# Kernel optimization log

Measured on AMD Instinct MI355X. Metric: run time of the kernel, lower is better.

## Reference

```python
import jax, jax.numpy as jnp
import numpy as np

C_IN = 256


def setup_inputs() -> dict:
    key = jax.random.key(0)
    ks = jax.random.split(key, 10)
    B, C, H, W = 1, C_IN, 96, 96
    Cq = C // 8
    s = 0.05
    return {
        "x": jax.random.normal(ks[0], (B, C, H, W), dtype=jnp.float32),
        "Wq": jax.random.normal(ks[1], (Cq, C), dtype=jnp.float32) * s,
        "bq": jax.random.normal(ks[2], (Cq,), dtype=jnp.float32) * s,
        "Wk": jax.random.normal(ks[3], (Cq, C), dtype=jnp.float32) * s,
        "bk": jax.random.normal(ks[4], (Cq,), dtype=jnp.float32) * s,
        "Wv": jax.random.normal(ks[5], (C, C), dtype=jnp.float32) * s,
        "bv": jax.random.normal(ks[6], (C,), dtype=jnp.float32) * s,
        "W6": jax.random.normal(ks[7], (C, C), dtype=jnp.float32) * s,
        "b6": jax.random.normal(ks[8], (C,), dtype=jnp.float32) * s,
        "gamma": jnp.ones((1,), dtype=jnp.float32),
    }


def reference(x, Wq, bq, Wk, bk, Wv, bv, W6, b6, gamma):
    # TRM forward (OFS just wraps it). 1x1 convs expressed as einsums.
    B, C, H, W = x.shape
    N = H * W
    scale = C ** -0.5  # 1 / sqrt(in_dim)
    xf = x.reshape(B, C, N)
    q = jnp.einsum('oc,bcn->bon', Wq, xf) + bq[None, :, None]   # (B, C/8, N)
    k = jnp.einsum('oc,bcn->bon', Wk, xf) + bk[None, :, None]   # (B, C/8, N)
    v = jnp.einsum('oc,bcn->bon', Wv, xf) + bv[None, :, None]   # (B, C,   N)
    # energy[b,n,m] = sum_c q[b,c,n] * k[b,c,m]  -> full spatial attention (B,N,N)
    energy = jnp.einsum('bcn,bcm->bnm', q, k)
    att = jax.nn.softmax(energy, axis=-1)
    # out[b,c,n] = sum_m v[b,c,m] * att[b,n,m]
    out = jnp.einsum('bcm,bnm->bcn', v, att)                    # (B, C, N)
    # torch: out.permute(2,0,1) -> (N,B,C); max/mean over C; sum; mean over B
    out_co = out.max(axis=1) + out.mean(axis=1)                 # (B, N)
    x_co = out_co.mean(axis=0).reshape(B, -1) * scale           # valid because B == 1
    x_co = jax.nn.softmax(x_co, axis=-1).reshape(B, 1, H, W)    # spatial gate
    gated = x * x_co
    y = jnp.einsum('oc,bchw->bohw', W6, gated) + b6[None, :, None, None]
    return gamma * y + x + y
```

## Files before the change

kernel.cpp:

```cpp
#include <hip/hip_runtime.h>

#define N 9216
#define CIN 256
#define DQ 32
#define NT 144
#define LOG2E 1.44269504088896340736f

typedef short short8 __attribute__((ext_vector_type(8)));
typedef float floatx4 __attribute__((ext_vector_type(4)));
typedef unsigned short ushort_t;

__device__ __forceinline__ ushort_t f2bf(float f) {
  union { float f; unsigned u; } a; a.f = f;
  unsigned u = a.u;
  u += 0x7fffu + ((u >> 16) & 1u);
  return (ushort_t)(u >> 16);
}
__device__ __forceinline__ float bf2f(ushort_t h) {
  union { unsigned u; float f; } a; a.u = ((unsigned)h) << 16;
  return a.f;
}

__global__ __launch_bounds__(256) void qkv_kernel(
    const float* __restrict__ x,
    const float* __restrict__ Wq, const float* __restrict__ bq,
    const float* __restrict__ Wk, const float* __restrict__ bk,
    const float* __restrict__ Wv, const float* __restrict__ bv,
    ushort_t* __restrict__ qT, ushort_t* __restrict__ kT,
    ushort_t* __restrict__ vG)
{
  __shared__ float xs[64][68];
  const int t = threadIdx.x;
  const int n0 = blockIdx.x * 64;
  const int oc = blockIdx.y;
  const int i = t >> 4, j = t & 15;
  const int o0 = oc * 64 + i * 4;

  const float* Wrow[4];
  float bias[4];
#pragma unroll
  for (int r = 0; r < 4; ++r) {
    const int o = o0 + r;
    if (oc == 0) {
      if (o < 32) { Wrow[r] = Wq + o * CIN;        bias[r] = bq[o]; }
      else        { Wrow[r] = Wk + (o - 32) * CIN; bias[r] = bk[o - 32]; }
    } else        { Wrow[r] = Wv + (o - 64) * CIN; bias[r] = bv[o - 64]; }
  }

  float acc[4][4] = {};
  for (int cc = 0; cc < 4; ++cc) {
    {
      const int row = t >> 2, cq = t & 3;
      const float* src = x + (size_t)(cc * 64 + row) * N + n0 + cq * 16;
      float4 a0 = *(const float4*)(src + 0);
      float4 a1 = *(const float4*)(src + 4);
      float4 a2 = *(const float4*)(src + 8);
      float4 a3 = *(const float4*)(src + 12);
      float* dst = &xs[row][cq * 16];
      *(float4*)(dst + 0) = a0; *(float4*)(dst + 4)  = a1;
      *(float4*)(dst + 8) = a2; *(float4*)(dst + 12) = a3;
    }
    __syncthreads();
#pragma unroll 2
    for (int k4 = 0; k4 < 16; ++k4) {
      float4 wv4[4];
#pragma unroll
      for (int r = 0; r < 4; ++r)
        wv4[r] = *(const float4*)(Wrow[r] + cc * 64 + k4 * 4);
#pragma unroll
      for (int kk = 0; kk < 4; ++kk) {
        float4 xv = *(const float4*)&xs[k4 * 4 + kk][j * 4];
#pragma unroll
        for (int r = 0; r < 4; ++r) {
          const float wval = ((const float*)&wv4[r])[kk];
          acc[r][0] += wval * xv.x;
          acc[r][1] += wval * xv.y;
          acc[r][2] += wval * xv.z;
          acc[r][3] += wval * xv.w;
        }
      }
    }
    __syncthreads();
  }

#pragma unroll
  for (int r = 0; r < 4; ++r) {
    const int o = o0 + r;
#pragma unroll
    for (int c = 0; c < 4; ++c) {
      const int n = n0 + j * 4 + c;
      const float val = acc[r][c] + bias[r];
      if (oc == 0) {
        if (o < 32) qT[(size_t)n * DQ + o]        = f2bf(val * LOG2E);
        else        kT[(size_t)n * DQ + (o - 32)] = f2bf(val);
      } else        vG[(size_t)(o - 64) * N + n]  = f2bf(val);
    }
  }
}

__global__ __launch_bounds__(256, 2) void attn_kernel(
    const ushort_t* __restrict__ qT, const ushort_t* __restrict__ kT,
    const ushort_t* __restrict__ vG,
    ushort_t* __restrict__ Opart, float* __restrict__ lpart,
    int sliceIters)
{
  __shared__ ushort_t Pb[2][64][36];

  const int t = threadIdx.x;
  const int w = t >> 6;
  const int lane = t & 63;
  const int quad = lane >> 4;
  const int l15 = lane & 15;
  const int nt = blockIdx.x;
  const int s  = blockIdx.y;
  const int n0 = nt * 64;
  const int mbase = s * sliceIters * 32;
  const int cw = w * 64;

  short8 aq = *(const short8*)(qT + (size_t)(n0 + 16 * w + l15) * DQ + 8 * quad);

  floatx4 acc[4][4];
#pragma unroll
  for (int a2 = 0; a2 < 4; ++a2)
#pragma unroll
    for (int b2 = 0; b2 < 4; ++b2)
      acc[a2][b2] = (floatx4){0.f, 0.f, 0.f, 0.f};
  float lsum[4] = {0.f, 0.f, 0.f, 0.f};
  const floatx4 z4 = {0.f, 0.f, 0.f, 0.f};

  for (int it = 0; it < sliceIters; ++it) {
    const int m0 = mbase + it * 32;

    short8 kb0 = *(const short8*)(kT + (size_t)(m0 + l15) * DQ + 8 * quad);
    short8 kb1 = *(const short8*)(kT + (size_t)(m0 + 16 + l15) * DQ + 8 * quad);
    floatx4 s0 = __builtin_amdgcn_mfma_f32_16x16x32_bf16(aq, kb0, z4, 0, 0, 0);
    floatx4 s1 = __builtin_amdgcn_mfma_f32_16x16x32_bf16(aq, kb1, z4, 0, 0, 0);

    const ushort_t* vb = vG + (size_t)m0 + 8 * quad;
    short8 av0 = *(const short8*)(vb + (size_t)(cw +  0 + l15) * N);
    short8 av1 = *(const short8*)(vb + (size_t)(cw + 16 + l15) * N);
    short8 av2 = *(const short8*)(vb + (size_t)(cw + 32 + l15) * N);
    short8 av3 = *(const short8*)(vb + (size_t)(cw + 48 + l15) * N);

    ushort_t* pb = &Pb[it & 1][0][0];
#pragma unroll
    for (int r = 0; r < 4; ++r) {
      float p0 = exp2f(s0[r]);
      float p1 = exp2f(s1[r]);
      lsum[r] += p0 + p1;
      const int row = 16 * w + 4 * quad + r;
      pb[row * 36 + l15]      = f2bf(p0);
      pb[row * 36 + 16 + l15] = f2bf(p1);
    }
    __syncthreads();

#pragma unroll
    for (int b2 = 0; b2 < 4; ++b2) {
      const ushort_t* pr = pb + (b2 * 16 + l15) * 36 + 8 * quad;
      union { uint2 u2[2]; short8 v; } u;
      u.u2[0] = *(const uint2*)(pr);
      u.u2[1] = *(const uint2*)(pr + 4);
      const short8 pf = u.v;
      acc[0][b2] = __builtin_amdgcn_mfma_f32_16x16x32_bf16(av0, pf, acc[0][b2], 0, 0, 0);
      acc[1][b2] = __builtin_amdgcn_mfma_f32_16x16x32_bf16(av1, pf, acc[1][b2], 0, 0, 0);
      acc[2][b2] = __builtin_amdgcn_mfma_f32_16x16x32_bf16(av2, pf, acc[2][b2], 0, 0, 0);
      acc[3][b2] = __builtin_amdgcn_mfma_f32_16x16x32_bf16(av3, pf, acc[3][b2], 0, 0, 0);
    }
  }

#pragma unroll
  for (int r = 0; r < 4; ++r) {
    float v = lsum[r];
    v += __shfl_xor(v, 1);
    v += __shfl_xor(v, 2);
    v += __shfl_xor(v, 4);
    v += __shfl_xor(v, 8);
    lsum[r] = v;
  }
  if (l15 == 0) {
#pragma unroll
    for (int r = 0; r < 4; ++r)
      lpart[(size_t)s * N + n0 + 16 * w + 4 * quad + r] = lsum[r];
  }

  const size_t base = ((size_t)s * NT + nt) * 256;
#pragma unroll
  for (int a2 = 0; a2 < 4; ++a2)
#pragma unroll
    for (int b2 = 0; b2 < 4; ++b2)
#pragma unroll
      for (int r = 0; r < 4; ++r) {
        const int c  = cw + a2 * 16 + 4 * quad + r;
        const int nl = b2 * 16 + l15;
        Opart[(base + c) * 64 + nl] = f2bf(acc[a2][b2][r]);
      }
}

__global__ __launch_bounds__(256) void cco_partial(
    const ushort_t* __restrict__ Opart,
    float* __restrict__ pmax, float* __restrict__ psum, int nsl)
{
  const int nt = blockIdx.x, cy = blockIdx.y;
  const int t = threadIdx.x;
  const int n = t & 63, ci = t >> 6;
  float mx = -3.4e38f, sm = 0.f;
#pragma unroll
  for (int k = 0; k < 8; ++k) {
    const int c = cy * 32 + ci + 4 * k;
    float val = 0.f;
#pragma unroll 8
    for (int s2 = 0; s2 < nsl; ++s2)
      val += bf2f(Opart[(((size_t)s2 * NT + nt) * 256 + c) * 64 + n]);
    mx = fmaxf(mx, val);
    sm += val;
  }
  __shared__ float rmx[4][64], rsm[4][64];
  rmx[ci][n] = mx; rsm[ci][n] = sm;
  __syncthreads();
  if (t < 64) {
    const float m2 = fmaxf(fmaxf(rmx[0][t], rmx[1][t]), fmaxf(rmx[2][t], rmx[3][t]));
    const float s2 = rsm[0][t] + rsm[1][t] + rsm[2][t] + rsm[3][t];
    pmax[(size_t)cy * N + nt * 64 + t] = m2;
    psum[(size_t)cy * N + nt * 64 + t] = s2;
  }
}

__global__ __launch_bounds__(256) void cco_final(
    const float* __restrict__ pmax, const float* __restrict__ psum,
    const float* __restrict__ lpart, float* __restrict__ out_co, int nsl)
{
  const int n = blockIdx.x * 256 + threadIdx.x;
  float m = -3.4e38f, s = 0.f, l = 0.f;
#pragma unroll
  for (int g = 0; g < 8; ++g) {
    m = fmaxf(m, pmax[(size_t)g * N + n]);
    s += psum[(size_t)g * N + n];
  }
#pragma unroll 8
  for (int s3 = 0; s3 < nsl; ++s3) l += lpart[(size_t)s3 * N + n];
  out_co[n] = (m + s * (1.0f / 256.0f)) / l;
}

__global__ __launch_bounds__(1024) void gate_kernel(
    const float* __restrict__ out_co, float* __restrict__ x_co)
{
  const int t = threadIdx.x;
  float z[9];
#pragma unroll
  for (int i2 = 0; i2 < 9; ++i2) z[i2] = out_co[t + 1024 * i2] * 0.0625f;
  float mx = z[0];
#pragma unroll
  for (int i2 = 1; i2 < 9; ++i2) mx = fmaxf(mx, z[i2]);
  for (int off = 32; off > 0; off >>= 1) mx = fmaxf(mx, __shfl_xor(mx, off));
  __shared__ float redm[16], reds[16];
  const int wv = t >> 6, ln = t & 63;
  if (ln == 0) redm[wv] = mx;
  __syncthreads();
  mx = redm[0];
#pragma unroll
  for (int i2 = 1; i2 < 16; ++i2) mx = fmaxf(mx, redm[i2]);

  float e[9]; float sm = 0.f;
#pragma unroll
  for (int i2 = 0; i2 < 9; ++i2) { e[i2] = exp2f((z[i2] - mx) * LOG2E); sm += e[i2]; }
  for (int off = 32; off > 0; off >>= 1) sm += __shfl_xor(sm, off);
  if (ln == 0) reds[wv] = sm;
  __syncthreads();
  sm = 0.f;
#pragma unroll
  for (int i2 = 0; i2 < 16; ++i2) sm += reds[i2];
  const float inv = 1.0f / sm;
#pragma unroll
  for (int i2 = 0; i2 < 9; ++i2) x_co[t + 1024 * i2] = e[i2] * inv;
}

__global__ __launch_bounds__(256) void final_kernel(
    const float* __restrict__ x, const float* __restrict__ W6,
    const float* __restrict__ b6, const float* __restrict__ gamma,
    const float* __restrict__ x_co, float* __restrict__ out)
{
  __shared__ float xs[64][68];
  const int t = threadIdx.x;
  const int n0 = blockIdx.x * 64;
  const int i = t >> 4, j = t & 15;
  const int o0 = blockIdx.y * 64 + i * 4;

  float acc[4][4] = {};
  for (int cc = 0; cc < 4; ++cc) {
    {
      const int row = t >> 2, cq = t & 3;
      const float* src = x + (size_t)(cc * 64 + row) * N + n0 + cq * 16;
      float4 a0 = *(const float4*)(src + 0);
      float4 a1 = *(const float4*)(src + 4);
      float4 a2 = *(const float4*)(src + 8);
      float4 a3 = *(const float4*)(src + 12);
      float* dst = &xs[row][cq * 16];
      *(float4*)(dst + 0) = a0; *(float4*)(dst + 4)  = a1;
      *(float4*)(dst + 8) = a2; *(float4*)(dst + 12) = a3;
    }
    __syncthreads();
#pragma unroll 2
    for (int k4 = 0; k4 < 16; ++k4) {
      float4 wv4[4];
#pragma unroll
      for (int r = 0; r < 4; ++r)
        wv4[r] = *(const float4*)(W6 + (size_t)(o0 + r) * CIN + cc * 64 + k4 * 4);
#pragma unroll
      for (int kk = 0; kk < 4; ++kk) {
        float4 xv = *(const float4*)&xs[k4 * 4 + kk][j * 4];
#pragma unroll
        for (int r = 0; r < 4; ++r) {
          const float wval = ((const float*)&wv4[r])[kk];
          acc[r][0] += wval * xv.x;
          acc[r][1] += wval * xv.y;
          acc[r][2] += wval * xv.z;
          acc[r][3] += wval * xv.w;
        }
      }
    }
    __syncthreads();
  }

  const float g1 = 1.0f + gamma[0];
  const float4 xc = *(const float4*)(x_co + n0 + j * 4);
#pragma unroll
  for (int r = 0; r < 4; ++r) {
    const int o = o0 + r;
    const float bv6 = b6[o];
    const float4 xrow = *(const float4*)(x + (size_t)o * N + n0 + j * 4);
    float4 res;
    res.x = xrow.x + g1 * (xc.x * acc[r][0] + bv6);
    res.y = xrow.y + g1 * (xc.y * acc[r][1] + bv6);
    res.z = xrow.z + g1 * (xc.z * acc[r][2] + bv6);
    res.w = xrow.w + g1 * (xc.w * acc[r][3] + bv6);
    *(float4*)(out + (size_t)o * N + n0 + j * 4) = res;
  }
}

extern "C" void kernel_launch(void* const* d_in, const int* in_sizes, int n_in,
                              void* d_out, int out_size, void* d_ws, size_t ws_size,
                              hipStream_t stream)
{
  const float* x     = (const float*)d_in[0];
  const float* Wq    = (const float*)d_in[1];
  const float* bq    = (const float*)d_in[2];
  const float* Wk    = (const float*)d_in[3];
  const float* bk    = (const float*)d_in[4];
  const float* Wv    = (const float*)d_in[5];
  const float* bv    = (const float*)d_in[6];
  const float* W6    = (const float*)d_in[7];
  const float* b6    = (const float*)d_in[8];
  const float* gamma = (const float*)d_in[9];
  float* out = (float*)d_out;

  const size_t fixed = (size_t)N * DQ * 2 * 2
                     + (size_t)CIN * N * 2
                     + (size_t)N * 4 * 2
                     + (size_t)8 * N * 4 * 2;
  int nsl = 8;
  size_t need8 = fixed + (size_t)8 * NT * 256 * 64 * 2 + (size_t)8 * N * 4;
  if (ws_size < need8) nsl = 4;
  const int sliceIters = (N / nsl) / 32;

  char* ws = (char*)d_ws;
  const size_t OFF_QT = 0;
  const size_t OFF_KT = OFF_QT + (size_t)N * DQ * 2;
  const size_t OFF_V  = OFF_KT + (size_t)N * DQ * 2;
  const size_t OFF_OP = OFF_V  + (size_t)CIN * N * 2;
  const size_t OFF_LP = OFF_OP + (size_t)nsl * NT * 256 * 64 * 2;
  const size_t OFF_PM = OFF_LP + (size_t)nsl * N * 4;
  const size_t OFF_PS = OFF_PM + (size_t)8 * N * 4;
  const size_t OFF_OC = OFF_PS + (size_t)8 * N * 4;
  const size_t OFF_XC = OFF_OC + (size_t)N * 4;

  ushort_t* qT     = (ushort_t*)(ws + OFF_QT);
  ushort_t* kT     = (ushort_t*)(ws + OFF_KT);
  ushort_t* vG     = (ushort_t*)(ws + OFF_V);
  ushort_t* Opart  = (ushort_t*)(ws + OFF_OP);
  float*    lpart  = (float*)(ws + OFF_LP);
  float*    pmax   = (float*)(ws + OFF_PM);
  float*    psum   = (float*)(ws + OFF_PS);
  float*    out_co = (float*)(ws + OFF_OC);
  float*    x_co   = (float*)(ws + OFF_XC);

  qkv_kernel<<<dim3(NT, 5), 256, 0, stream>>>(x, Wq, bq, Wk, bk, Wv, bv, qT, kT, vG);
  attn_kernel<<<dim3(NT, nsl), 256, 0, stream>>>(qT, kT, vG, Opart, lpart, sliceIters);
  cco_partial<<<dim3(NT, 8), 256, 0, stream>>>(Opart, pmax, psum, nsl);
  cco_final<<<N / 256, 256, 0, stream>>>(pmax, psum, lpart, out_co, nsl);
  gate_kernel<<<1, 1024, 0, stream>>>(out_co, x_co);
  final_kernel<<<dim3(NT, 4), 256, 0, stream>>>(x, W6, b6, gamma, x_co, out);
}
```

Before: 255.4 us.

## Widen attention key tile to 64 and fold cco_final into gate kernel

```diff
diff --git a/kernel.cpp b/kernel.cpp
--- a/kernel.cpp
+++ b/kernel.cpp
@@ -98,13 +98,13 @@
   }
 }
 
-__global__ __launch_bounds__(256, 2) void attn_kernel(
+__global__ __launch_bounds__(256, 3) void attn_kernel(
     const ushort_t* __restrict__ qT, const ushort_t* __restrict__ kT,
     const ushort_t* __restrict__ vG,
     ushort_t* __restrict__ Opart, float* __restrict__ lpart,
-    int sliceIters)
-{
-  __shared__ ushort_t Pb[2][64][36];
+    int mIters)
+{
+  __shared__ ushort_t Pb[2][64][68];
 
   const int t = threadIdx.x;
   const int w = t >> 6;
@@ -114,7 +114,7 @@
   const int nt = blockIdx.x;
   const int s  = blockIdx.y;
   const int n0 = nt * 64;
-  const int mbase = s * sliceIters * 32;
+  const int mbase = s * mIters * 64;
   const int cw = w * 64;
 
   short8 aq = *(const short8*)(qT + (size_t)(n0 + 16 * w + l15) * DQ + 8 * quad);
@@ -128,43 +128,64 @@
   float lsum[4] = {0.f, 0.f, 0.f, 0.f};
   const floatx4 z4 = {0.f, 0.f, 0.f, 0.f};
 
-  for (int it = 0; it < sliceIters; ++it) {
-    const int m0 = mbase + it * 32;
-
-    short8 kb0 = *(const short8*)(kT + (size_t)(m0 + l15) * DQ + 8 * quad);
-    short8 kb1 = *(const short8*)(kT + (size_t)(m0 + 16 + l15) * DQ + 8 * quad);
-    floatx4 s0 = __builtin_amdgcn_mfma_f32_16x16x32_bf16(aq, kb0, z4, 0, 0, 0);
-    floatx4 s1 = __builtin_amdgcn_mfma_f32_16x16x32_bf16(aq, kb1, z4, 0, 0, 0);
+  for (int it = 0; it < mIters; ++it) {
+    const int m0 = mbase + it * 64;
+
+    const ushort_t* kr = kT + (size_t)(m0 + l15) * DQ + 8 * quad;
+    short8 kb0 = *(const short8*)(kr);
+    short8 kb1 = *(const short8*)(kr + 16 * DQ);
+    short8 kb2 = *(const short8*)(kr + 32 * DQ);
+    short8 kb3 = *(const short8*)(kr + 48 * DQ);
 
     const ushort_t* vb = vG + (size_t)m0 + 8 * quad;
     short8 av0 = *(const short8*)(vb + (size_t)(cw +  0 + l15) * N);
     short8 av1 = *(const short8*)(vb + (size_t)(cw + 16 + l15) * N);
     short8 av2 = *(const short8*)(vb + (size_t)(cw + 32 + l15) * N);
     short8 av3 = *(const short8*)(vb + (size_t)(cw + 48 + l15) * N);
+    short8 av4 = *(const short8*)(vb + (size_t)(cw +  0 + l15) * N + 32);
+    short8 av5 = *(const short8*)(vb + (size_t)(cw + 16 + l15) * N + 32);
+    short8 av6 = *(const short8*)(vb + (size_t)(cw + 32 + l15) * N + 32);
+    short8 av7 = *(const short8*)(vb + (size_t)(cw + 48 + l15) * N + 32);
+
+    floatx4 s0 = __builtin_amdgcn_mfma_f32_16x16x32_bf16(aq, kb0, z4, 0, 0, 0);
+    floatx4 s1 = __builtin_amdgcn_mfma_f32_16x16x32_bf16(aq, kb1, z4, 0, 0, 0);
+    floatx4 s2 = __builtin_amdgcn_mfma_f32_16x16x32_bf16(aq, kb2, z4, 0, 0, 0);
+    floatx4 s3 = __builtin_amdgcn_mfma_f32_16x16x32_bf16(aq, kb3, z4, 0, 0, 0);
 
     ushort_t* pb = &Pb[it & 1][0][0];
 #pragma unroll
     for (int r = 0; r < 4; ++r) {
       float p0 = exp2f(s0[r]);
       float p1 = exp2f(s1[r]);
-      lsum[r] += p0 + p1;
-      const int row = 16 * w + 4 * quad + r;
-      pb[row * 36 + l15]      = f2bf(p0);
-      pb[row * 36 + 16 + l15] = f2bf(p1);
+      float p2 = exp2f(s2[r]);
+      float p3 = exp2f(s3[r]);
+      lsum[r] += (p0 + p1) + (p2 + p3);
+      ushort_t* pr = pb + (16 * w + 4 * quad + r) * 68 + l15;
+      pr[0]  = f2bf(p0);
+      pr[16] = f2bf(p1);
+      pr[32] = f2bf(p2);
+      pr[48] = f2bf(p3);
     }
     __syncthreads();
 
 #pragma unroll
     for (int b2 = 0; b2 < 4; ++b2) {
-      const ushort_t* pr = pb + (b2 * 16 + l15) * 36 + 8 * quad;
-      union { uint2 u2[2]; short8 v; } u;
-      u.u2[0] = *(const uint2*)(pr);
-      u.u2[1] = *(const uint2*)(pr + 4);
-      const short8 pf = u.v;
-      acc[0][b2] = __builtin_amdgcn_mfma_f32_16x16x32_bf16(av0, pf, acc[0][b2], 0, 0, 0);
-      acc[1][b2] = __builtin_amdgcn_mfma_f32_16x16x32_bf16(av1, pf, acc[1][b2], 0, 0, 0);
-      acc[2][b2] = __builtin_amdgcn_mfma_f32_16x16x32_bf16(av2, pf, acc[2][b2], 0, 0, 0);
-      acc[3][b2] = __builtin_amdgcn_mfma_f32_16x16x32_bf16(av3, pf, acc[3][b2], 0, 0, 0);
+      const ushort_t* pr = pb + (b2 * 16 + l15) * 68 + 8 * quad;
+      union { uint2 u2[2]; short8 v; } u0, u1;
+      u0.u2[0] = *(const uint2*)(pr);
+      u0.u2[1] = *(const uint2*)(pr + 4);
+      u1.u2[0] = *(const uint2*)(pr + 32);
+      u1.u2[1] = *(const uint2*)(pr + 36);
+      const short8 pf0 = u0.v;
+      const short8 pf1 = u1.v;
+      acc[0][b2] = __builtin_amdgcn_mfma_f32_16x16x32_bf16(av0, pf0, acc[0][b2], 0, 0, 0);
+      acc[1][b2] = __builtin_amdgcn_mfma_f32_16x16x32_bf16(av1, pf0, acc[1][b2], 0, 0, 0);
+      acc[2][b2] = __builtin_amdgcn_mfma_f32_16x16x32_bf16(av2, pf0, acc[2][b2], 0, 0, 0);
+      acc[3][b2] = __builtin_amdgcn_mfma_f32_16x16x32_bf16(av3, pf0, acc[3][b2], 0, 0, 0);
+      acc[0][b2] = __builtin_amdgcn_mfma_f32_16x16x32_bf16(av4, pf1, acc[0][b2], 0, 0, 0);
+      acc[1][b2] = __builtin_amdgcn_mfma_f32_16x16x32_bf16(av5, pf1, acc[1][b2], 0, 0, 0);
+      acc[2][b2] = __builtin_amdgcn_mfma_f32_16x16x32_bf16(av6, pf1, acc[2][b2], 0, 0, 0);
+      acc[3][b2] = __builtin_amdgcn_mfma_f32_16x16x32_bf16(av7, pf1, acc[3][b2], 0, 0, 0);
     }
   }
 
@@ -225,29 +246,25 @@
   }
 }
 
-__global__ __launch_bounds__(256) void cco_final(
+__global__ __launch_bounds__(1024) void gate_kernel(
     const float* __restrict__ pmax, const float* __restrict__ psum,
-    const float* __restrict__ lpart, float* __restrict__ out_co, int nsl)
-{
-  const int n = blockIdx.x * 256 + threadIdx.x;
-  float m = -3.4e38f, s = 0.f, l = 0.f;
-#pragma unroll
-  for (int g = 0; g < 8; ++g) {
-    m = fmaxf(m, pmax[(size_t)g * N + n]);
-    s += psum[(size_t)g * N + n];
-  }
-#pragma unroll 8
-  for (int s3 = 0; s3 < nsl; ++s3) l += lpart[(size_t)s3 * N + n];
-  out_co[n] = (m + s * (1.0f / 256.0f)) / l;
-}
-
-__global__ __launch_bounds__(1024) void gate_kernel(
-    const float* __restrict__ out_co, float* __restrict__ x_co)
+    const float* __restrict__ lpart, float* __restrict__ x_co, int nsl)
 {
   const int t = threadIdx.x;
   float z[9];
 #pragma unroll
-  for (int i2 = 0; i2 < 9; ++i2) z[i2] = out_co[t + 1024 * i2] * 0.0625f;
+  for (int i2 = 0; i2 < 9; ++i2) {
+    const int n = t + 1024 * i2;
+    float m = -3.4e38f, s = 0.f, l = 0.f;
+#pragma unroll
+    for (int g = 0; g < 8; ++g) {
+      m = fmaxf(m, pmax[(size_t)g * N + n]);
+      s += psum[(size_t)g * N + n];
+    }
+#pragma unroll 8
+    for (int s3 = 0; s3 < nsl; ++s3) l += lpart[(size_t)s3 * N + n];
+    z[i2] = ((m + s * (1.0f / 256.0f)) / l) * 0.0625f;
+  }
   float mx = z[0];
 #pragma unroll
   for (int i2 = 1; i2 < 9; ++i2) mx = fmaxf(mx, z[i2]);
@@ -355,12 +372,12 @@
 
   const size_t fixed = (size_t)N * DQ * 2 * 2
                      + (size_t)CIN * N * 2
-                     + (size_t)N * 4 * 2
+                     + (size_t)N * 4
                      + (size_t)8 * N * 4 * 2;
   int nsl = 8;
   size_t need8 = fixed + (size_t)8 * NT * 256 * 64 * 2 + (size_t)8 * N * 4;
   if (ws_size < need8) nsl = 4;
-  const int sliceIters = (N / nsl) / 32;
+  const int mIters = (N / nsl) / 64;
 
   char* ws = (char*)d_ws;
   const size_t OFF_QT = 0;
@@ -370,8 +387,7 @@
   const size_t OFF_LP = OFF_OP + (size_t)nsl * NT * 256 * 64 * 2;
   const size_t OFF_PM = OFF_LP + (size_t)nsl * N * 4;
   const size_t OFF_PS = OFF_PM + (size_t)8 * N * 4;
-  const size_t OFF_OC = OFF_PS + (size_t)8 * N * 4;
-  const size_t OFF_XC = OFF_OC + (size_t)N * 4;
+  const size_t OFF_XC = OFF_PS + (size_t)8 * N * 4;
 
   ushort_t* qT     = (ushort_t*)(ws + OFF_QT);
   ushort_t* kT     = (ushort_t*)(ws + OFF_KT);
@@ -380,13 +396,11 @@
   float*    lpart  = (float*)(ws + OFF_LP);
   float*    pmax   = (float*)(ws + OFF_PM);
   float*    psum   = (float*)(ws + OFF_PS);
-  float*    out_co = (float*)(ws + OFF_OC);
   float*    x_co   = (float*)(ws + OFF_XC);
 
   qkv_kernel<<<dim3(NT, 5), 256, 0, stream>>>(x, Wq, bq, Wk, bk, Wv, bv, qT, kT, vG);
-  attn_kernel<<<dim3(NT, nsl), 256, 0, stream>>>(qT, kT, vG, Opart, lpart, sliceIters);
+  attn_kernel<<<dim3(NT, nsl), 256, 0, stream>>>(qT, kT, vG, Opart, lpart, mIters);
   cco_partial<<<dim3(NT, 8), 256, 0, stream>>>(Opart, pmax, psum, nsl);
-  cco_final<<<N / 256, 256, 0, stream>>>(pmax, psum, lpart, out_co, nsl);
-  gate_kernel<<<1, 1024, 0, stream>>>(out_co, x_co);
+  gate_kernel<<<1, 1024, 0, stream>>>(pmax, psum, lpart, x_co, nsl);
   final_kernel<<<dim3(NT, 4), 256, 0, stream>>>(x, W6, b6, gamma, x_co, out);
 }
```

Result: slower. 278.9 us (+9.2%).
